# Optimization experiments

Hardware: AMD Instinct MI355X
Metric: run time of the kernel (lower is better)

Reference implementation:

```python
import jax, jax.numpy as jnp
import numpy as np

N = 50000      # nodes
E = 500000     # edges
IN = 128       # input feature dim
HID = 64       # hidden per-head dim
CLS = 64       # num classes
SLOPE = 0.2    # leaky_relu negative slope


def _gat_layer(x, W, al, ar, src, dst):
    """One GATConv: project, per-edge score, edge-softmax over dst, weighted aggregate.
    x: [N, Din], W: [Din, H*F], al/ar: [H, F]. Returns [N, H, F]."""
    H, F = al.shape
    n = x.shape[0]
    feat = (x @ W).reshape(n, H, F)                      # [N,H,F]
    el = jnp.einsum('nhf,hf->nh', feat, al)              # [N,H]
    er = jnp.einsum('nhf,hf->nh', feat, ar)              # [N,H]
    e = el[src] + er[dst]                                # u_add_v -> [E,H]
    e = jnp.where(e >= 0, e, SLOPE * e)                  # leaky_relu
    # edge_softmax over destination nodes (numerically stable)
    m = jax.lax.stop_gradient(jax.ops.segment_max(e, dst, num_segments=n))
    ex = jnp.exp(e - m[dst])
    denom = jax.ops.segment_sum(ex, dst, num_segments=n)
    a = ex / denom[dst]                                  # [E,H]
    # u_mul_e + sum aggregation
    out = jax.ops.segment_sum(feat[src] * a[:, :, None], dst, num_segments=n)
    return out                                           # [N,H,F]


def setup_inputs() -> dict:
    key = jax.random.key(0)
    ks = jax.random.split(key, 12)
    s = 0.05  # xavier-ish scale
    x = jax.random.normal(ks[0], (N, IN), jnp.float32)
    src = jax.random.randint(ks[1], (E,), 0, N)
    dst = jax.random.randint(ks[2], (E,), 0, N)
    W1 = jax.random.normal(ks[3], (IN, 4 * HID), jnp.float32) * s
    al1 = jax.random.normal(ks[4], (4, HID), jnp.float32) * s
    ar1 = jax.random.normal(ks[5], (4, HID), jnp.float32) * s
    W2 = jax.random.normal(ks[6], (4 * HID, 4 * HID), jnp.float32) * s
    al2 = jax.random.normal(ks[7], (4, HID), jnp.float32) * s
    ar2 = jax.random.normal(ks[8], (4, HID), jnp.float32) * s
    W3 = jax.random.normal(ks[9], (4 * HID, CLS), jnp.float32) * s
    al3 = jax.random.normal(ks[10], (1, CLS), jnp.float32) * s
    ar3 = jax.random.normal(ks[11], (1, CLS), jnp.float32) * s
    res_W3 = jax.random.normal(jax.random.fold_in(key, 99), (4 * HID, CLS), jnp.float32) * s
    return {"x": x, "W1": W1, "al1": al1, "ar1": ar1, "W2": W2, "al2": al2,
            "ar2": ar2, "W3": W3, "al3": al3, "ar3": ar3, "res_W3": res_W3,
            "src": src, "dst": dst}


def reference(x, W1, al1, ar1, W2, al2, ar2, W3, al3, ar3, res_W3, src, dst):
    # layer 0: no residual, elu activation, flatten heads
    h = _gat_layer(x, W1, al1, ar1, src, dst)            # [N,4,64]
    h = jax.nn.elu(h).reshape(N, -1)                     # [N,256]
    # layer 1: residual is Identity (in_dst 256 == 4*64), elu, flatten
    h1 = _gat_layer(h, W2, al2, ar2, src, dst)           # [N,4,64]
    h1 = h1 + h.reshape(N, 4, HID)                       # residual (Identity)
    h = jax.nn.elu(h1).reshape(N, -1)                    # [N,256]
    # layer 2: residual Linear 256->64, no activation, mean over heads
    h2 = _gat_layer(h, W3, al3, ar3, src, dst)           # [N,1,64]
    h2 = h2 + (h @ res_W3).reshape(N, 1, CLS)            # residual fc
    logits = h2.mean(axis=1)                             # [N,64]
    return logits
```

## Files before the change

### kernel.cpp

```cpp
#include <hip/hip_runtime.h>
#include <hip/hip_bf16.h>
#include <math.h>

#define SLOPE 0.2f

typedef __attribute__((ext_vector_type(8))) short short8;
typedef __attribute__((ext_vector_type(4))) float f32x4;
typedef __attribute__((ext_vector_type(4))) int   i32x4;

static __device__ __forceinline__ float leakyf(float x) { return x >= 0.f ? x : SLOPE * x; }
static __device__ __forceinline__ float bflo(unsigned u) { return __builtin_bit_cast(float, u << 16); }
static __device__ __forceinline__ float bfhi(unsigned u) { return __builtin_bit_cast(float, u & 0xffff0000u); }
static __device__ __forceinline__ unsigned short f2bf(float f) {
    unsigned u = __builtin_bit_cast(unsigned, f);
    return (unsigned short)((u + 0x7fff + ((u >> 16) & 1)) >> 16);
}

struct __align__(8) us4 { unsigned short a, b, c, d; };


__global__ __launch_bounds__(256) void prep(const float* __restrict__ W1,
                                            const float* __restrict__ W2,
                                            const float* __restrict__ W3,
                                            const float* __restrict__ rW3,
                                            unsigned short* __restrict__ W1t,
                                            unsigned short* __restrict__ W2t,
                                            unsigned short* __restrict__ W3c,
                                            int* __restrict__ counts,
                                            int* __restrict__ bflag, int n) {
    int b = blockIdx.x;
    if (b < 512) {
        int i = b * 256 + threadIdx.x;
        const float* W; unsigned short* Wt; int K, lNc, idx; bool permK;
        if (i < 32768)       { W = W1;  Wt = W1t;            K = 128; lNc = 8; idx = i;          permK = false; }
        else if (i < 98304)  { W = W2;  Wt = W2t;            K = 256; lNc = 8; idx = i - 32768;  permK = true; }
        else if (i < 114688) { W = W3;  Wt = W3c;            K = 256; lNc = 6; idx = i - 98304;  permK = true; }
        else                 { W = rW3; Wt = W3c + 64 * 256; K = 256; lNc = 6; idx = i - 114688; permK = true; }
        int k = idx >> lNc, nn = idx & ((1 << lNc) - 1);
        int kp = permK ? ((k & ~63) | (((k & 15) << 2) | ((k & 63) >> 4))) : k;
        Wt[nn * K + kp] = f2bf(W[idx]);
    } else {
        if (b == 512 && threadIdx.x < 64) bflag[threadIdx.x] = 0;
        int idx = (b - 512) * 256 + threadIdx.x;
        if (idx < n) counts[idx] = 0;
    }
}

template<bool A_F32>
static __device__ __forceinline__ void gemm_l12_body(int bid, const void* __restrict__ Av,
                                                     const unsigned short* __restrict__ Wt,
                                                     unsigned short* __restrict__ outb,
                                                     const float* __restrict__ al,
                                                     const float* __restrict__ ar,
                                                     float* __restrict__ el,
                                                     float* __restrict__ er,
                                                     int M, int K) {
    const int lane = threadIdx.x & 63;
    const int wid = threadIdx.x >> 6;
    const int rlo = lane & 15;
    const int q = lane >> 4;
    const int kg = q * 8;
    const int m0 = bid * 64;
    const int cbase = wid * 64;

    f32x4 acc[4][4];
#pragma unroll
    for (int mf = 0; mf < 4; ++mf)
#pragma unroll
        for (int nf = 0; nf < 4; ++nf) acc[mf][nf] = (f32x4){0.f, 0.f, 0.f, 0.f};

    for (int k0 = 0; k0 < K; k0 += 32) {
        short8 a[4];
#pragma unroll
        for (int mf = 0; mf < 4; ++mf) {
            int r = m0 + mf * 16 + rlo;
            if (r >= M) r = M - 1;
            if (A_F32) {
                const float* ap = (const float*)Av + (size_t)r * K + k0 + kg;
                float4 f0 = *(const float4*)ap;
                float4 f1 = *(const float4*)(ap + 4);
                short8 t;
                t[0] = f2bf(f0.x); t[1] = f2bf(f0.y); t[2] = f2bf(f0.z); t[3] = f2bf(f0.w);
                t[4] = f2bf(f1.x); t[5] = f2bf(f1.y); t[6] = f2bf(f1.z); t[7] = f2bf(f1.w);
                a[mf] = t;
            } else {
                a[mf] = *(const short8*)((const unsigned short*)Av + (size_t)r * K + k0 + kg);
            }
        }
#pragma unroll
        for (int nf = 0; nf < 4; ++nf) {
            short8 b = *(const short8*)(Wt + (size_t)(cbase + nf * 16 + rlo) * K + k0 + kg);
#pragma unroll
            for (int mf = 0; mf < 4; ++mf)
                acc[mf][nf] = __builtin_amdgcn_mfma_f32_16x16x32_bf16(a[mf], b, acc[mf][nf], 0, 0, 0);
        }
    }

    float alv[4], arv[4];
#pragma unroll
    for (int nf = 0; nf < 4; ++nf) {
        alv[nf] = al[cbase + nf * 16 + rlo];
        arv[nf] = ar[cbase + nf * 16 + rlo];
    }

#pragma unroll
    for (int mf = 0; mf < 4; ++mf) {
#pragma unroll
        for (int reg = 0; reg < 4; ++reg) {
            int r = m0 + mf * 16 + q * 4 + reg;
            float pl = 0.f, pr = 0.f;
#pragma unroll
            for (int nf = 0; nf < 4; ++nf) {
                pl += acc[mf][nf][reg] * alv[nf];
                pr += acc[mf][nf][reg] * arv[nf];
            }
#pragma unroll
            for (int off = 1; off < 16; off <<= 1) {
                pl += __shfl_xor(pl, off);
                pr += __shfl_xor(pr, off);
            }
            if (rlo == 0 && r < M) {
                el[(size_t)r * 4 + wid] = pl;
                er[(size_t)r * 4 + wid] = pr;
            }
            if (r < M) {
                us4 o = {f2bf(acc[mf][0][reg]), f2bf(acc[mf][1][reg]),
                         f2bf(acc[mf][2][reg]), f2bf(acc[mf][3][reg])};
                *(us4*)(outb + (size_t)r * 256 + cbase + rlo * 4) = o;
            }
        }
    }
}

template<bool A_F32>
__global__ __launch_bounds__(256) void gemm_l12(const void* __restrict__ Av,
                                                const unsigned short* __restrict__ Wt,
                                                unsigned short* __restrict__ outb,
                                                const float* __restrict__ al,
                                                const float* __restrict__ ar,
                                                float* __restrict__ el,
                                                float* __restrict__ er, int M, int K) {
    gemm_l12_body<A_F32>(blockIdx.x, Av, Wt, outb, al, ar, el, er, M, K);
}

__global__ __launch_bounds__(256) void gemm1_scatter(const float* __restrict__ x,
                                                     const unsigned short* __restrict__ W1t,
                                                     unsigned short* __restrict__ featb,
                                                     const float* __restrict__ al,
                                                     const float* __restrict__ ar,
                                                     float* __restrict__ el,
                                                     float* __restrict__ er,
                                                     int M, int K, int gemm_blocks,
                                                     const int* __restrict__ src,
                                                     const int* __restrict__ dst,
                                                     int* __restrict__ cursor,
                                                     int* __restrict__ csr_src,
                                                     int* __restrict__ csr_dst, int E) {
    int b = blockIdx.x;
    if (b < gemm_blocks) {
        gemm_l12_body<true>(b, x, W1t, featb, al, ar, el, er, M, K);
    } else {
        int i = (b - gemm_blocks) * 256 + threadIdx.x;
        if (i < E) {
            int d = dst[i];
            int pos = atomicAdd(&cursor[d], 1);
            csr_src[pos] = src[i];
            csr_dst[pos] = d;
        }
    }
}

__global__ __launch_bounds__(256) void gemm_l3(const unsigned short* __restrict__ A,
                                               const unsigned short* __restrict__ Wt,
                                               unsigned short* __restrict__ featb,
                                               float* __restrict__ resf,
                                               const float* __restrict__ al,
                                               const float* __restrict__ ar,
                                               float* __restrict__ el,
                                               float* __restrict__ er, int M) {
    const int K = 256;
    const int lane = threadIdx.x & 63;
    const int wid = threadIdx.x >> 6;
    const int rlo = lane & 15;
    const int q = lane >> 4;
    const int kg = q * 8;
    const int m0 = blockIdx.x * 128 + (wid >> 1) * 64;
    const int ch = wid & 1;
    const int cbase = ch * 64;

    f32x4 acc[4][4];
#pragma unroll
    for (int mf = 0; mf < 4; ++mf)
#pragma unroll
        for (int nf = 0; nf < 4; ++nf) acc[mf][nf] = (f32x4){0.f, 0.f, 0.f, 0.f};

    for (int k0 = 0; k0 < K; k0 += 32) {
        short8 a[4];
#pragma unroll
        for (int mf = 0; mf < 4; ++mf) {
            int r = m0 + mf * 16 + rlo;
            if (r >= M) r = M - 1;
            a[mf] = *(const short8*)(A + (size_t)r * K + k0 + kg);
        }
#pragma unroll
        for (int nf = 0; nf < 4; ++nf) {
            short8 b = *(const short8*)(Wt + (size_t)(cbase + nf * 16 + rlo) * K + k0 + kg);
#pragma unroll
            for (int mf = 0; mf < 4; ++mf)
                acc[mf][nf] = __builtin_amdgcn_mfma_f32_16x16x32_bf16(a[mf], b, acc[mf][nf], 0, 0, 0);
        }
    }

    float alv[4], arv[4];
    if (ch == 0) {
#pragma unroll
        for (int nf = 0; nf < 4; ++nf) {
            alv[nf] = al[nf * 16 + rlo];
            arv[nf] = ar[nf * 16 + rlo];
        }
    }

#pragma unroll
    for (int mf = 0; mf < 4; ++mf) {
#pragma unroll
        for (int reg = 0; reg < 4; ++reg) {
            int r = m0 + mf * 16 + q * 4 + reg;
            if (ch == 0) {
                float pl = 0.f, pr = 0.f;
#pragma unroll
                for (int nf = 0; nf < 4; ++nf) {
                    pl += acc[mf][nf][reg] * alv[nf];
                    pr += acc[mf][nf][reg] * arv[nf];
                }
#pragma unroll
                for (int off = 1; off < 16; off <<= 1) {
                    pl += __shfl_xor(pl, off);
                    pr += __shfl_xor(pr, off);
                }
                if (rlo == 0 && r < M) { el[r] = pl; er[r] = pr; }
                if (r < M) {
                    us4 o = {f2bf(acc[mf][0][reg]), f2bf(acc[mf][1][reg]),
                             f2bf(acc[mf][2][reg]), f2bf(acc[mf][3][reg])};
                    *(us4*)(featb + (size_t)r * 64 + rlo * 4) = o;
                }
            } else if (r < M) {
                float4 o = {acc[mf][0][reg], acc[mf][1][reg], acc[mf][2][reg], acc[mf][3][reg]};
                *(float4*)(resf + (size_t)r * 64 + rlo * 4) = o;
            }
        }
    }
}

__global__ void hist_kernel(const int* __restrict__ dst, int* __restrict__ counts, int e) {
    int i = blockIdx.x * blockDim.x + threadIdx.x;
    if (i < e) atomicAdd(&counts[dst[i]], 1);
}

__global__ __launch_bounds__(1024) void scan_lookback(const int* __restrict__ counts,
                                                      int* __restrict__ offsets,
                                                      int* __restrict__ cursor,
                                                      int* __restrict__ bsum,
                                                      int* __restrict__ bflag, int n, int e) {
    __shared__ int ws[16];
    __shared__ int base_s;
    int tid = threadIdx.x, lane = tid & 63, wid = tid >> 6, bid = blockIdx.x;
    int idx = bid * 1024 + tid;
    int v = (idx < n) ? counts[idx] : 0;
    int s = v;
#pragma unroll
    for (int off = 1; off < 64; off <<= 1) {
        int t = __shfl_up(s, off);
        if (lane >= off) s += t;
    }
    if (lane == 63) ws[wid] = s;
    __syncthreads();
    if (tid < 16) {
        int w2 = ws[tid];
#pragma unroll
        for (int off = 1; off < 16; off <<= 1) {
            int t = __shfl_up(w2, off);
            if (tid >= off) w2 += t;
        }
        ws[tid] = w2;
    }
    __syncthreads();
    int local_ex = (wid ? ws[wid - 1] : 0) + s - v;
    if (tid == 0) {
        __hip_atomic_store(&bsum[bid], ws[15], __ATOMIC_RELAXED, __HIP_MEMORY_SCOPE_AGENT);
        __hip_atomic_store(&bflag[bid], 1, __ATOMIC_RELEASE, __HIP_MEMORY_SCOPE_AGENT);
    }
    if (wid == 0) {
        int acc = 0;
        for (int p = lane; p < bid; p += 64) {
            while (__hip_atomic_load(&bflag[p], __ATOMIC_ACQUIRE, __HIP_MEMORY_SCOPE_AGENT) == 0) {}
            acc += __hip_atomic_load(&bsum[p], __ATOMIC_RELAXED, __HIP_MEMORY_SCOPE_AGENT);
        }
#pragma unroll
        for (int off = 32; off > 0; off >>= 1) acc += __shfl_xor(acc, off);
        if (lane == 0) base_s = acc;
    }
    __syncthreads();
    int val = base_s + local_ex;
    if (idx < n) {
        offsets[idx] = val;
        cursor[idx] = val;
    }
    if (idx == 0) offsets[n] = e;
}

template<int H>
__global__ __launch_bounds__(256) void edge_scores(const int* __restrict__ csr_src,
                                                   const int* __restrict__ csr_dst,
                                                   const float* __restrict__ el,
                                                   const float* __restrict__ er,
                                                   float* __restrict__ w, int E) {
    int e4 = (blockIdx.x * 256 + threadIdx.x) * 4;
    if (e4 >= E) return;
    i32x4 s = *(const i32x4*)(csr_src + e4);
    i32x4 d = *(const i32x4*)(csr_dst + e4);
    if (H == 4) {
        float4 o0, o1, o2, o3;
        float* op[4] = {&o0.x, &o1.x, &o2.x, &o3.x};
#pragma unroll
        for (int j = 0; j < 4; ++j) {
            float4 l = *(const float4*)(el + (size_t)s[j] * 4);
            float4 r = *(const float4*)(er + (size_t)d[j] * 4);
            op[0][j] = __expf(fminf(leakyf(l.x + r.x), 80.f));
            op[1][j] = __expf(fminf(leakyf(l.y + r.y), 80.f));
            op[2][j] = __expf(fminf(leakyf(l.z + r.z), 80.f));
            op[3][j] = __expf(fminf(leakyf(l.w + r.w), 80.f));
        }
        *(float4*)(w + 0 * (size_t)E + e4) = o0;
        *(float4*)(w + 1 * (size_t)E + e4) = o1;
        *(float4*)(w + 2 * (size_t)E + e4) = o2;
        *(float4*)(w + 3 * (size_t)E + e4) = o3;
    } else {
        float4 o;
#pragma unroll
        for (int j = 0; j < 4; ++j)
            (&o.x)[j] = __expf(fminf(leakyf(el[s[j]] + er[d[j]]), 80.f));
        *(float4*)(w + e4) = o;
    }
}

template<int RES, int ACT>
__global__ __launch_bounds__(256) void gat_agg4(const unsigned short* __restrict__ fp,
                                                const float* __restrict__ wbuf,
                                                const int* __restrict__ offsets,
                                                const int* __restrict__ csr_src,
                                                const unsigned short* __restrict__ resid,
                                                unsigned short* __restrict__ outb,
                                                int n, int E) {
    int wv = threadIdx.x >> 6;
    int lane = threadIdx.x & 63;
    int half = lane >> 5;
    int sub = lane & 31;
    int node = blockIdx.x * 8 + wv * 2 + half;

    int e0 = 0, e1 = 0;
    if (node < n) { e0 = offsets[node]; e1 = offsets[node + 1]; }
    int cnt = e1 - e0;
    int ocnt = __shfl_xor(cnt, 32);
    int mc = cnt > ocnt ? cnt : ocnt;

    const float* wb = wbuf + (size_t)(sub >> 3) * E;

    float den = 0.f;
    float acc[8] = {0.f, 0.f, 0.f, 0.f, 0.f, 0.f, 0.f, 0.f};

    for (int t = 0; t < mc; t += 8) {
        i32x4 sv0, sv1;
        f32x4 wv0, wv1;
        __builtin_memcpy(&sv0, csr_src + e0 + t, 16);
        __builtin_memcpy(&sv1, csr_src + e0 + t + 4, 16);
        __builtin_memcpy(&wv0, wb + e0 + t, 16);
        __builtin_memcpy(&wv1, wb + e0 + t + 4, 16);
        int s[8];
        float w[8];
#pragma unroll
        for (int j = 0; j < 8; ++j) {
            bool ok = (t + j) < cnt;
            int sj = (j < 4) ? sv0[j] : sv1[j - 4];
            float wj = (j < 4) ? wv0[j] : wv1[j - 4];
            s[j] = ok ? sj : 0;
            w[j] = ok ? wj : 0.f;
        }
        uint4 u[8];
#pragma unroll
        for (int j = 0; j < 8; ++j)
            u[j] = *(const uint4*)(fp + (size_t)s[j] * 256 + sub * 8);
#pragma unroll
        for (int j = 0; j < 8; ++j) {
            den += w[j];
            acc[0] += w[j] * bflo(u[j].x);
            acc[1] += w[j] * bfhi(u[j].x);
            acc[2] += w[j] * bflo(u[j].y);
            acc[3] += w[j] * bfhi(u[j].y);
            acc[4] += w[j] * bflo(u[j].z);
            acc[5] += w[j] * bfhi(u[j].z);
            acc[6] += w[j] * bflo(u[j].w);
            acc[7] += w[j] * bfhi(u[j].w);
        }
    }

    if (node >= n) return;

    float inv = den > 0.f ? 1.f / den : 0.f;
    float v[8];
#pragma unroll
    for (int i = 0; i < 8; ++i) v[i] = acc[i] * inv;

    if (RES == 1) {
        uint4 ru = *(const uint4*)(resid + (size_t)node * 256 + sub * 8);
        v[0] += bflo(ru.x); v[1] += bfhi(ru.x);
        v[2] += bflo(ru.y); v[3] += bfhi(ru.y);
        v[4] += bflo(ru.z); v[5] += bfhi(ru.z);
        v[6] += bflo(ru.w); v[7] += bfhi(ru.w);
    }
    if (ACT == 1) {
#pragma unroll
        for (int i = 0; i < 8; ++i) v[i] = v[i] > 0.f ? v[i] : __expf(v[i]) - 1.f;
    }
    uint4 o;
    o.x = (unsigned)f2bf(v[0]) | ((unsigned)f2bf(v[1]) << 16);
    o.y = (unsigned)f2bf(v[2]) | ((unsigned)f2bf(v[3]) << 16);
    o.z = (unsigned)f2bf(v[4]) | ((unsigned)f2bf(v[5]) << 16);
    o.w = (unsigned)f2bf(v[6]) | ((unsigned)f2bf(v[7]) << 16);
    *(uint4*)(outb + (size_t)node * 256 + sub * 8) = o;
}

__global__ __launch_bounds__(256) void gat_agg1(const unsigned short* __restrict__ fp,
                                                const float* __restrict__ wbuf,
                                                const int* __restrict__ offsets,
                                                const int* __restrict__ csr_src,
                                                const float* __restrict__ resf,
                                                float* __restrict__ outv, int n, int E) {
    int wv = threadIdx.x >> 6;
    int lane = threadIdx.x & 63;
    int sub = lane & 15;
    int node = blockIdx.x * 16 + wv * 4 + (lane >> 4);

    int e0 = 0, e1 = 0;
    if (node < n) { e0 = offsets[node]; e1 = offsets[node + 1]; }
    int cnt = e1 - e0;
    int m1 = __shfl_xor(cnt, 16);
    int mc = cnt > m1 ? cnt : m1;
    int m2 = __shfl_xor(mc, 32);
    mc = mc > m2 ? mc : m2;

    float den = 0.f;
    float acc[4] = {0.f, 0.f, 0.f, 0.f};

    for (int t = 0; t < mc; t += 8) {
        i32x4 sv0, sv1;
        f32x4 wv0, wv1;
        __builtin_memcpy(&sv0, csr_src + e0 + t, 16);
        __builtin_memcpy(&sv1, csr_src + e0 + t + 4, 16);
        __builtin_memcpy(&wv0, wbuf + e0 + t, 16);
        __builtin_memcpy(&wv1, wbuf + e0 + t + 4, 16);
        int s[8];
        float w[8];
#pragma unroll
        for (int j = 0; j < 8; ++j) {
            bool ok = (t + j) < cnt;
            int sj = (j < 4) ? sv0[j] : sv1[j - 4];
            float wj = (j < 4) ? wv0[j] : wv1[j - 4];
            s[j] = ok ? sj : 0;
            w[j] = ok ? wj : 0.f;
        }
        uint2 u[8];
#pragma unroll
        for (int j = 0; j < 8; ++j)
            u[j] = *(const uint2*)(fp + (size_t)s[j] * 64 + sub * 4);
#pragma unroll
        for (int j = 0; j < 8; ++j) {
            den += w[j];
            acc[0] += w[j] * bflo(u[j].x);
            acc[1] += w[j] * bfhi(u[j].x);
            acc[2] += w[j] * bflo(u[j].y);
            acc[3] += w[j] * bfhi(u[j].y);
        }
    }

    if (node >= n) return;

    float inv = den > 0.f ? 1.f / den : 0.f;
    float4 rv = *(const float4*)(resf + (size_t)node * 64 + sub * 4);
    float v[4];
    v[0] = acc[0] * inv + rv.x;
    v[1] = acc[1] * inv + rv.y;
    v[2] = acc[2] * inv + rv.z;
    v[3] = acc[3] * inv + rv.w;

#pragma unroll
    for (int i = 0; i < 4; ++i) {
        int p = sub * 4 + i;
        int c = (p & 3) * 16 + (p >> 2);
        outv[(size_t)node * 64 + c] = v[i];
    }
}

extern "C" void kernel_launch(void* const* d_in, const int* in_sizes, int n_in,
                              void* d_out, int out_size, void* d_ws, size_t ws_size,
                              hipStream_t stream) {
    const float* x      = (const float*)d_in[0];
    const float* W1     = (const float*)d_in[1];
    const float* al1    = (const float*)d_in[2];
    const float* ar1    = (const float*)d_in[3];
    const float* W2     = (const float*)d_in[4];
    const float* al2    = (const float*)d_in[5];
    const float* ar2    = (const float*)d_in[6];
    const float* W3     = (const float*)d_in[7];
    const float* al3    = (const float*)d_in[8];
    const float* ar3    = (const float*)d_in[9];
    const float* res_W3 = (const float*)d_in[10];
    const int*   src    = (const int*)d_in[11];
    const int*   dst    = (const int*)d_in[12];

    const int N = in_sizes[0] / 128;
    const int E = in_sizes[11];

    float* out = (float*)d_out;

    unsigned short* featb = (unsigned short*)d_ws;
    unsigned short* h1    = featb + (size_t)N * 256;
    unsigned short* h2    = h1 + (size_t)N * 256;
    unsigned short* W1t   = h2 + (size_t)N * 256;
    unsigned short* W2t   = W1t + 256 * 128;
    unsigned short* W3c   = W2t + 256 * 256;
    float* resf = (float*)(W3c + 128 * 256);
    float* el   = resf + (size_t)N * 64;
    float* er   = el + (size_t)N * 4;
    float* wbuf = er + (size_t)N * 4;
    int* offsets = (int*)(wbuf + (size_t)E * 4);
    int* cursor  = offsets + (N + 8);
    int* csr_src = cursor + N;
    int* csr_dst = csr_src + E + 64;
    int* bsums   = csr_dst + E;
    int* bflag   = bsums + 64;

    const int T = 256;
    const int scan_blocks = (N + 1023) / 1024;
    const int edge_blocks = (E + T - 1) / T;
    const int zero_blocks = (N + 255) / 256;
    const int es_blocks = (E / 4 + T - 1) / T;

    int gemm12_blocks = (N + 63) / 64;
    int gemm3_blocks = (N + 127) / 128;
    int agg4_blocks = (N + 7) / 8;
    int agg1_blocks = (N + 15) / 16;

    prep<<<512 + zero_blocks, T, 0, stream>>>(W1, W2, W3, res_W3, W1t, W2t, W3c, cursor, bflag, N);
    hist_kernel<<<edge_blocks, T, 0, stream>>>(dst, cursor, E);
    scan_lookback<<<scan_blocks, 1024, 0, stream>>>(cursor, offsets, cursor, bsums, bflag, N, E);
    gemm1_scatter<<<gemm12_blocks + edge_blocks, T, 0, stream>>>(x, W1t, featb, al1, ar1, el, er,
                                                                 N, 128, gemm12_blocks,
                                                                 src, dst, cursor, csr_src, csr_dst, E);
    edge_scores<4><<<es_blocks, T, 0, stream>>>(csr_src, csr_dst, el, er, wbuf, E);
    gat_agg4<0, 1><<<agg4_blocks, T, 0, stream>>>(featb, wbuf, offsets, csr_src, nullptr, h1, N, E);
    gemm_l12<false><<<gemm12_blocks, T, 0, stream>>>(h1, W2t, featb, al2, ar2, el, er, N, 256);
    edge_scores<4><<<es_blocks, T, 0, stream>>>(csr_src, csr_dst, el, er, wbuf, E);
    gat_agg4<1, 1><<<agg4_blocks, T, 0, stream>>>(featb, wbuf, offsets, csr_src, h1, h2, N, E);
    gemm_l3<<<gemm3_blocks, T, 0, stream>>>(h2, W3c, featb, resf, al3, ar3, el, er, N);
    edge_scores<1><<<es_blocks, T, 0, stream>>>(csr_src, csr_dst, el, er, wbuf, E);
    gat_agg1<<<agg1_blocks, T, 0, stream>>>(featb, wbuf, offsets, csr_src, resf, out, N, E);
}
```

Baseline: 273.9 us.

## Interleave CSR src/dst into int2 array and fuse histogram with layer-1 GEMM

Stores CSR source and destination indices as interleaved int2 pairs, so a single scatter store writes both and edge_scores reads one vector stream instead of two. The dst histogram now runs inside the first GEMM launch, and the atomic scatter becomes its own kernel after the scan. This keeps the kernel count the same but moves the GEMM to overlap with the histogram rather than the scatter. The cost is that the aggregation kernels now read twice the index bytes, since they fetch dst values they never use.

```diff
diff --git a/kernel.cpp b/kernel.cpp
--- a/kernel.cpp
+++ b/kernel.cpp
@@ -143,30 +143,22 @@
     gemm_l12_body<A_F32>(blockIdx.x, Av, Wt, outb, al, ar, el, er, M, K);
 }
 
-__global__ __launch_bounds__(256) void gemm1_scatter(const float* __restrict__ x,
-                                                     const unsigned short* __restrict__ W1t,
-                                                     unsigned short* __restrict__ featb,
-                                                     const float* __restrict__ al,
-                                                     const float* __restrict__ ar,
-                                                     float* __restrict__ el,
-                                                     float* __restrict__ er,
-                                                     int M, int K, int gemm_blocks,
-                                                     const int* __restrict__ src,
-                                                     const int* __restrict__ dst,
-                                                     int* __restrict__ cursor,
-                                                     int* __restrict__ csr_src,
-                                                     int* __restrict__ csr_dst, int E) {
+__global__ __launch_bounds__(256) void gemm1_hist(const float* __restrict__ x,
+                                                  const unsigned short* __restrict__ W1t,
+                                                  unsigned short* __restrict__ featb,
+                                                  const float* __restrict__ al,
+                                                  const float* __restrict__ ar,
+                                                  float* __restrict__ el,
+                                                  float* __restrict__ er,
+                                                  int M, int K, int gemm_blocks,
+                                                  const int* __restrict__ dst,
+                                                  int* __restrict__ counts, int E) {
     int b = blockIdx.x;
     if (b < gemm_blocks) {
         gemm_l12_body<true>(b, x, W1t, featb, al, ar, el, er, M, K);
     } else {
         int i = (b - gemm_blocks) * 256 + threadIdx.x;
-        if (i < E) {
-            int d = dst[i];
-            int pos = atomicAdd(&cursor[d], 1);
-            csr_src[pos] = src[i];
-            csr_dst[pos] = d;
-        }
+        if (i < E) atomicAdd(&counts[dst[i]], 1);
     }
 }
 
@@ -251,11 +243,6 @@
     }
 }
 
-__global__ void hist_kernel(const int* __restrict__ dst, int* __restrict__ counts, int e) {
-    int i = blockIdx.x * blockDim.x + threadIdx.x;
-    if (i < e) atomicAdd(&counts[dst[i]], 1);
-}
-
 __global__ __launch_bounds__(1024) void scan_lookback(const int* __restrict__ counts,
                                                       int* __restrict__ offsets,
                                                       int* __restrict__ cursor,
@@ -308,16 +295,27 @@
     if (idx == 0) offsets[n] = e;
 }
 
+__global__ void scatter_sd(const int* __restrict__ src, const int* __restrict__ dst,
+                           int* __restrict__ cursor, int2* __restrict__ csr_sd, int e) {
+    int i = blockIdx.x * blockDim.x + threadIdx.x;
+    if (i < e) {
+        int d = dst[i];
+        int pos = atomicAdd(&cursor[d], 1);
+        csr_sd[pos] = make_int2(src[i], d);
+    }
+}
+
 template<int H>
-__global__ __launch_bounds__(256) void edge_scores(const int* __restrict__ csr_src,
-                                                   const int* __restrict__ csr_dst,
+__global__ __launch_bounds__(256) void edge_scores(const int2* __restrict__ csr_sd,
                                                    const float* __restrict__ el,
                                                    const float* __restrict__ er,
                                                    float* __restrict__ w, int E) {
     int e4 = (blockIdx.x * 256 + threadIdx.x) * 4;
     if (e4 >= E) return;
-    i32x4 s = *(const i32x4*)(csr_src + e4);
-    i32x4 d = *(const i32x4*)(csr_dst + e4);
+    i32x4 p0 = *(const i32x4*)(csr_sd + e4);
+    i32x4 p1 = *(const i32x4*)(csr_sd + e4 + 2);
+    int s[4] = {p0[0], p0[2], p1[0], p1[2]};
+    int d[4] = {p0[1], p0[3], p1[1], p1[3]};
     if (H == 4) {
         float4 o0, o1, o2, o3;
         float* op[4] = {&o0.x, &o1.x, &o2.x, &o3.x};
@@ -347,7 +345,7 @@
 __global__ __launch_bounds__(256) void gat_agg4(const unsigned short* __restrict__ fp,
                                                 const float* __restrict__ wbuf,
                                                 const int* __restrict__ offsets,
-                                                const int* __restrict__ csr_src,
+                                                const int2* __restrict__ csr_sd,
                                                 const unsigned short* __restrict__ resid,
                                                 unsigned short* __restrict__ outb,
                                                 int n, int E) {
@@ -369,20 +367,22 @@
     float acc[8] = {0.f, 0.f, 0.f, 0.f, 0.f, 0.f, 0.f, 0.f};
 
     for (int t = 0; t < mc; t += 8) {
-        i32x4 sv0, sv1;
+        i32x4 p0, p1, p2, p3;
         f32x4 wv0, wv1;
-        __builtin_memcpy(&sv0, csr_src + e0 + t, 16);
-        __builtin_memcpy(&sv1, csr_src + e0 + t + 4, 16);
+        __builtin_memcpy(&p0, csr_sd + e0 + t, 16);
+        __builtin_memcpy(&p1, csr_sd + e0 + t + 2, 16);
+        __builtin_memcpy(&p2, csr_sd + e0 + t + 4, 16);
+        __builtin_memcpy(&p3, csr_sd + e0 + t + 6, 16);
         __builtin_memcpy(&wv0, wb + e0 + t, 16);
         __builtin_memcpy(&wv1, wb + e0 + t + 4, 16);
+        int sr[8] = {p0[0], p0[2], p1[0], p1[2], p2[0], p2[2], p3[0], p3[2]};
         int s[8];
         float w[8];
 #pragma unroll
         for (int j = 0; j < 8; ++j) {
             bool ok = (t + j) < cnt;
-            int sj = (j < 4) ? sv0[j] : sv1[j - 4];
             float wj = (j < 4) ? wv0[j] : wv1[j - 4];
-            s[j] = ok ? sj : 0;
+            s[j] = ok ? sr[j] : 0;
             w[j] = ok ? wj : 0.f;
         }
         uint4 u[8];
@@ -432,7 +432,7 @@
 __global__ __launch_bounds__(256) void gat_agg1(const unsigned short* __restrict__ fp,
                                                 const float* __restrict__ wbuf,
                                                 const int* __restrict__ offsets,
-                                                const int* __restrict__ csr_src,
+                                                const int2* __restrict__ csr_sd,
                                                 const float* __restrict__ resf,
                                                 float* __restrict__ outv, int n, int E) {
     int wv = threadIdx.x >> 6;
@@ -452,20 +452,22 @@
     float acc[4] = {0.f, 0.f, 0.f, 0.f};
 
     for (int t = 0; t < mc; t += 8) {
-        i32x4 sv0, sv1;
+        i32x4 p0, p1, p2, p3;
         f32x4 wv0, wv1;
-        __builtin_memcpy(&sv0, csr_src + e0 + t, 16);
-        __builtin_memcpy(&sv1, csr_src + e0 + t + 4, 16);
+        __builtin_memcpy(&p0, csr_sd + e0 + t, 16);
+        __builtin_memcpy(&p1, csr_sd + e0 + t + 2, 16);
+        __builtin_memcpy(&p2, csr_sd + e0 + t + 4, 16);
+        __builtin_memcpy(&p3, csr_sd + e0 + t + 6, 16);
         __builtin_memcpy(&wv0, wbuf + e0 + t, 16);
         __builtin_memcpy(&wv1, wbuf + e0 + t + 4, 16);
+        int sr[8] = {p0[0], p0[2], p1[0], p1[2], p2[0], p2[2], p3[0], p3[2]};
         int s[8];
         float w[8];
 #pragma unroll
         for (int j = 0; j < 8; ++j) {
             bool ok = (t + j) < cnt;
-            int sj = (j < 4) ? sv0[j] : sv1[j - 4];
             float wj = (j < 4) ? wv0[j] : wv1[j - 4];
-            s[j] = ok ? sj : 0;
+            s[j] = ok ? sr[j] : 0;
             w[j] = ok ? wj : 0.f;
         }
         uint2 u[8];
@@ -534,9 +536,8 @@
     float* wbuf = er + (size_t)N * 4;
     int* offsets = (int*)(wbuf + (size_t)E * 4);
     int* cursor  = offsets + (N + 8);
-    int* csr_src = cursor + N;
-    int* csr_dst = csr_src + E + 64;
-    int* bsums   = csr_dst + E;
+    int2* csr_sd = (int2*)(cursor + N);
+    int* bsums   = (int*)(csr_sd + E + 32);
     int* bflag   = bsums + 64;
 
     const int T = 256;
@@ -551,17 +552,16 @@
     int agg1_blocks = (N + 15) / 16;
 
     prep<<<512 + zero_blocks, T, 0, stream>>>(W1, W2, W3, res_W3, W1t, W2t, W3c, cursor, bflag, N);
-    hist_kernel<<<edge_blocks, T, 0, stream>>>(dst, cursor, E);
+    gemm1_hist<<<gemm12_blocks + edge_blocks, T, 0, stream>>>(x, W1t, featb, al1, ar1, el, er,
+                                                              N, 128, gemm12_blocks, dst, cursor, E);
     scan_lookback<<<scan_blocks, 1024, 0, stream>>>(cursor, offsets, cursor, bsums, bflag, N, E);
-    gemm1_scatter<<<gemm12_blocks + edge_blocks, T, 0, stream>>>(x, W1t, featb, al1, ar1, el, er,
-                                                                 N, 128, gemm12_blocks,
-                                                                 src, dst, cursor, csr_src, csr_dst, E);
-    edge_scores<4><<<es_blocks, T, 0, stream>>>(csr_src, csr_dst, el, er, wbuf, E);
-    gat_agg4<0, 1><<<agg4_blocks, T, 0, stream>>>(featb, wbuf, offsets, csr_src, nullptr, h1, N, E);
+    scatter_sd<<<edge_blocks, T, 0, stream>>>(src, dst, cursor, csr_sd, E);
+    edge_scores<4><<<es_blocks, T, 0, stream>>>(csr_sd, el, er, wbuf, E);
+    gat_agg4<0, 1><<<agg4_blocks, T, 0, stream>>>(featb, wbuf, offsets, csr_sd, nullptr, h1, N, E);
     gemm_l12<false><<<gemm12_blocks, T, 0, stream>>>(h1, W2t, featb, al2, ar2, el, er, N, 256);
-    edge_scores<4><<<es_blocks, T, 0, stream>>>(csr_src, csr_dst, el, er, wbuf, E);
-    gat_agg4<1, 1><<<agg4_blocks, T, 0, stream>>>(featb, wbuf, offsets, csr_src, h1, h2, N, E);
+    edge_scores<4><<<es_blocks, T, 0, stream>>>(csr_sd, el, er, wbuf, E);
+    gat_agg4<1, 1><<<agg4_blocks, T, 0, stream>>>(featb, wbuf, offsets, csr_sd, h1, h2, N, E);
     gemm_l3<<<gemm3_blocks, T, 0, stream>>>(h2, W3c, featb, resf, al3, ar3, el, er, N);
-    edge_scores<1><<<es_blocks, T, 0, stream>>>(csr_src, csr_dst, el, er, wbuf, E);
-    gat_agg1<<<agg1_blocks, T, 0, stream>>>(featb, wbuf, offsets, csr_src, resf, out, N, E);
-}
+    edge_scores<1><<<es_blocks, T, 0, stream>>>(csr_sd, el, er, wbuf, E);
+    gat_agg1<<<agg1_blocks, T, 0, stream>>>(featb, wbuf, offsets, csr_sd, resf, out, N, E);
+}
```

Result: faster. 263.5 us (-3.8%).
